# Kernel optimization log

Measured on AMD Instinct MI355X. Metric: run time of the kernel, lower is better.

## Reference

```python
import jax, jax.numpy as jnp
import numpy as np

DIM = 64     # qudit dimension (size of M)
WIRES = 3    # total qudits; full Hilbert dim D = DIM**WIRES = 262144
INDEX = 1    # wire the custom gate acts on
BATCH = 128  # number of state columns


def setup_inputs() -> dict:
    key = jax.random.key(0)
    k1, k2, k3, k4 = jax.random.split(key, 4)
    D = DIM ** WIRES
    return {
        "M_real": jax.random.normal(k1, (DIM, DIM), dtype=jnp.float32),
        "M_imag": jax.random.normal(k2, (DIM, DIM), dtype=jnp.float32),
        "x_real": jax.random.normal(k3, (D, BATCH), dtype=jnp.float32),
        "x_imag": jax.random.normal(k4, (D, BATCH), dtype=jnp.float32),
    }


def reference(M_real, M_imag, x_real, x_imag):
    # Original torch code builds U = I_{dim^index} (x) M (x) I_{dim^(wires-index-1)}
    # via iterative kron, then computes U @ x. Mathematically identical and
    # exponentially cheaper: reshape x to expose the target qudit axis and
    # contract M only along that axis (tensor-network style).
    M = jax.lax.complex(M_real, M_imag)          # (dim, dim) complex64
    x = jax.lax.complex(x_real, x_imag)          # (D, B) complex64
    B = x.shape[1]
    left = DIM ** INDEX                          # dims before target wire
    right = DIM ** (WIRES - INDEX - 1)           # dims after target wire
    xr = x.reshape(left, DIM, right, B)          # (a, j, r, b)
    y = jnp.einsum('ij,ajrb->airb', M, xr)       # apply M on the target axis
    return y.reshape(DIM ** WIRES, B)            # same as (kron U) @ x
```

## Files before the change

kernel.cpp:

```cpp
#include <hip/hip_runtime.h>

#define DIMQ   64
#define NCOLS  8192
#define SLAB   (DIMQ * NCOLS)
#define NA     64
#define DB     (NA * SLAB)

#define NT     128
#define TILES  8
#define NCG    8

typedef __attribute__((ext_vector_type(8))) __bf16 bf16x8;
typedef __attribute__((ext_vector_type(8))) unsigned short us8;
typedef __attribute__((ext_vector_type(4))) unsigned short us4;
typedef __attribute__((ext_vector_type(4))) float f32x4;

__device__ __forceinline__ unsigned short f2bf(float f) {
    unsigned u = __builtin_bit_cast(unsigned, f);
    unsigned r = u + 0x7fffu + ((u >> 16) & 1u);
    return (unsigned short)(r >> 16);
}

__device__ __forceinline__ int xsw(int row, int chunk) {
    return chunk ^ ((row >> 2) & 7) ^ ((row & 3) << 1);
}

__global__ __launch_bounds__(512, 4) void gate_real_kernel(
    const float* __restrict__ Mr, const float* __restrict__ Mi,
    const float* __restrict__ Xr, const float* __restrict__ Xi,
    float* __restrict__ Out)
{
    __shared__ alignas(16) unsigned char smem[32768];
    unsigned short* ldsX = (unsigned short*)smem;
    float* ldsO = (float*)smem;

    const int tid  = threadIdx.x;
    const int lane = tid & 63;
    const int w    = tid >> 6;
    const int l15  = lane & 15;
    const int q    = lane >> 4;
    const int it   = w & 3;
    const int nh   = w >> 2;

    const int a  = blockIdx.x >> 3;
    const int cg = blockIdx.x & 7;
    const size_t baseA = (size_t)a * SLAB;
    const int ncg0 = cg * (TILES * NT);

    bf16x8 fMr[2], fMni[2];
#pragma unroll
    for (int kb = 0; kb < 2; ++kb) {
        const int row = it * 16 + l15;
        const int col = kb * 32 + q * 8;
        const float* pr = Mr + row * DIMQ + col;
        const float* pi = Mi + row * DIMQ + col;
        us8 hr, hni;
#pragma unroll
        for (int j = 0; j < 8; ++j) {
            hr[j]  = f2bf(pr[j]);
            hni[j] = (unsigned short)(f2bf(pi[j]) ^ 0x8000u);
        }
        fMr[kb]  = __builtin_bit_cast(bf16x8, hr);
        fMni[kb] = __builtin_bit_cast(bf16x8, hni);
    }

    const int k0    = (tid >> 5) * 4;
    const int sn    = (tid & 31) * 4;
    const int chunk = k0 >> 3;
    const int ko4   = k0 & 4;

    f32x4 vr[4], vi[4];
    {
        const float* gr = Xr + baseA + (size_t)k0 * NCOLS + ncg0 + sn;
        const float* gi = Xi + baseA + (size_t)k0 * NCOLS + ncg0 + sn;
#pragma unroll
        for (int j = 0; j < 4; ++j)
            vr[j] = *reinterpret_cast<const f32x4*>(gr + (size_t)j * NCOLS);
#pragma unroll
        for (int j = 0; j < 4; ++j)
            vi[j] = *reinterpret_cast<const f32x4*>(gi + (size_t)j * NCOLS);
    }

    for (int t = 0; t < TILES; ++t) {
#pragma unroll
        for (int z = 0; z < 4; ++z) {
            const int row = sn + z;
            const int e   = row * 64 + xsw(row, chunk) * 8 + ko4;
            us4 hr, hi;
#pragma unroll
            for (int j = 0; j < 4; ++j) {
                hr[j] = f2bf(vr[j][z]);
                hi[j] = f2bf(vi[j][z]);
            }
            *reinterpret_cast<us4*>(&ldsX[e])        = hr;
            *reinterpret_cast<us4*>(&ldsX[8192 + e]) = hi;
        }

        if (t + 1 < TILES) {
            const float* gr = Xr + baseA + (size_t)k0 * NCOLS + ncg0 + (t + 1) * NT + sn;
            const float* gi = Xi + baseA + (size_t)k0 * NCOLS + ncg0 + (t + 1) * NT + sn;
#pragma unroll
            for (int j = 0; j < 4; ++j)
                vr[j] = *reinterpret_cast<const f32x4*>(gr + (size_t)j * NCOLS);
#pragma unroll
            for (int j = 0; j < 4; ++j)
                vi[j] = *reinterpret_cast<const f32x4*>(gi + (size_t)j * NCOLS);
        }
        __syncthreads();

        f32x4 acc[4];
#pragma unroll
        for (int nt = 0; nt < 4; ++nt) acc[nt] = f32x4{0, 0, 0, 0};
#pragma unroll
        for (int nt = 0; nt < 4; ++nt) {
#pragma unroll
            for (int kb = 0; kb < 2; ++kb) {
                const int row = (nh * 4 + nt) * 16 + l15;
                const int e   = row * 64 + xsw(row, kb * 4 + q) * 8;
                const bf16x8 bXr = __builtin_bit_cast(bf16x8,
                    *reinterpret_cast<const us8*>(&ldsX[e]));
                const bf16x8 bXi = __builtin_bit_cast(bf16x8,
                    *reinterpret_cast<const us8*>(&ldsX[8192 + e]));
                acc[nt] = __builtin_amdgcn_mfma_f32_16x16x32_bf16(fMr[kb],  bXr, acc[nt], 0, 0, 0);
                acc[nt] = __builtin_amdgcn_mfma_f32_16x16x32_bf16(fMni[kb], bXi, acc[nt], 0, 0, 0);
            }
        }
        __syncthreads();

#pragma unroll
        for (int nt = 0; nt < 4; ++nt) {
#pragma unroll
            for (int r = 0; r < 4; ++r) {
                const int row = it * 16 + q * 4 + r;
                const int col = nh * 64 + nt * 16 + l15;
                ldsO[row * 128 + (col ^ ((row & 7) << 2))] = acc[nt][r];
            }
        }
        __syncthreads();

        {
            const int ci = (tid & 31) * 4;
            const int r0 = tid >> 5;
            const int n0 = ncg0 + t * NT;
#pragma unroll
            for (int p = 0; p < 4; ++p) {
                const int row = p * 16 + r0;
                const int d   = ci ^ ((row & 7) << 2);
                const f32x4 v = *reinterpret_cast<const f32x4*>(&ldsO[row * 128 + d]);
                *reinterpret_cast<f32x4*>(Out + baseA + (size_t)row * NCOLS + n0 + ci) = v;
            }
        }
        __syncthreads();
    }
}

__device__ __forceinline__ void load_M_frags_full(
    const float* __restrict__ Mr, const float* __restrict__ Mi,
    int l15, int q, bf16x8 fMr[4][2], bf16x8 fMi[4][2])
{
#pragma unroll
    for (int it = 0; it < 4; ++it) {
#pragma unroll
        for (int kb = 0; kb < 2; ++kb) {
            const int row = it * 16 + l15;
            const int col = kb * 32 + q * 8;
            const float* pr = Mr + row * DIMQ + col;
            const float* pi = Mi + row * DIMQ + col;
            us8 hr, hi;
#pragma unroll
            for (int j = 0; j < 8; ++j) {
                hr[j] = f2bf(pr[j]);
                hi[j] = f2bf(pi[j]);
            }
            fMr[it][kb] = __builtin_bit_cast(bf16x8, hr);
            fMi[it][kb] = __builtin_bit_cast(bf16x8, hi);
        }
    }
}

__global__ __launch_bounds__(64, 2) void gate_cplx_kernel(
    const float* __restrict__ Mr, const float* __restrict__ Mi,
    const float* __restrict__ Xr, const float* __restrict__ Xi,
    float* __restrict__ Out)
{
    const int lane = threadIdx.x;
    const int l15  = lane & 15;
    const int q    = lane >> 4;

    bf16x8 fMr[4][2], fMi[4][2];
    load_M_frags_full(Mr, Mi, l15, q, fMr, fMi);

    const int bid = blockIdx.x;
    const int a   = bid >> 6;
    const int nch = bid & 63;
    const size_t baseA = (size_t)a * SLAB;

    for (int tt = 0; tt < 8; ++tt) {
        const int n0 = nch * 128 + tt * 16;
        f32x4 accR[4] = {f32x4{0,0,0,0}, f32x4{0,0,0,0}, f32x4{0,0,0,0}, f32x4{0,0,0,0}};
        f32x4 accI[4] = {f32x4{0,0,0,0}, f32x4{0,0,0,0}, f32x4{0,0,0,0}, f32x4{0,0,0,0}};

#pragma unroll
        for (int kb = 0; kb < 2; ++kb) {
            const int krow = kb * 32 + q * 8;
            const float* pr = Xr + baseA + (size_t)krow * NCOLS + n0 + l15;
            const float* pi = Xi + baseA + (size_t)krow * NCOLS + n0 + l15;
            float fr[8], fi[8];
#pragma unroll
            for (int j = 0; j < 8; ++j) {
                fr[j] = pr[(size_t)j * NCOLS];
                fi[j] = pi[(size_t)j * NCOLS];
            }
            us8 hr, hi, hni;
#pragma unroll
            for (int j = 0; j < 8; ++j) {
                hr[j] = f2bf(fr[j]);
                const unsigned short tbf = f2bf(fi[j]);
                hi[j]  = tbf;
                hni[j] = (unsigned short)(tbf ^ 0x8000u);
            }
            const bf16x8 bXr  = __builtin_bit_cast(bf16x8, hr);
            const bf16x8 bXi  = __builtin_bit_cast(bf16x8, hi);
            const bf16x8 bXni = __builtin_bit_cast(bf16x8, hni);

#pragma unroll
            for (int it = 0; it < 4; ++it) {
                accR[it] = __builtin_amdgcn_mfma_f32_16x16x32_bf16(fMr[it][kb], bXr,  accR[it], 0, 0, 0);
                accR[it] = __builtin_amdgcn_mfma_f32_16x16x32_bf16(fMi[it][kb], bXni, accR[it], 0, 0, 0);
                accI[it] = __builtin_amdgcn_mfma_f32_16x16x32_bf16(fMr[it][kb], bXi,  accI[it], 0, 0, 0);
                accI[it] = __builtin_amdgcn_mfma_f32_16x16x32_bf16(fMi[it][kb], bXr,  accI[it], 0, 0, 0);
            }
        }

#pragma unroll
        for (int it = 0; it < 4; ++it) {
#pragma unroll
            for (int r = 0; r < 4; ++r) {
                const int i = it * 16 + q * 4 + r;
                const size_t cidx = baseA + (size_t)i * NCOLS + n0 + l15;
                float2 v;
                v.x = accR[it][r];
                v.y = accI[it][r];
                reinterpret_cast<float2*>(Out)[cidx] = v;
            }
        }
    }
}

extern "C" void kernel_launch(void* const* d_in, const int* in_sizes, int n_in,
                              void* d_out, int out_size, void* d_ws, size_t ws_size,
                              hipStream_t stream) {
    const float* Mr = (const float*)d_in[0];
    const float* Mi = (const float*)d_in[1];
    const float* Xr = (const float*)d_in[2];
    const float* Xi = (const float*)d_in[3];
    float* Out = (float*)d_out;

    if (out_size >= 2 * DB) {
        dim3 grid(NA * 64);
        dim3 block(64);
        gate_cplx_kernel<<<grid, block, 0, stream>>>(Mr, Mi, Xr, Xi, Out);
    } else {
        dim3 grid(NA * NCG);
        dim3 block(512);
        gate_real_kernel<<<grid, block, 0, stream>>>(Mr, Mi, Xr, Xi, Out);
    }
}
```

Baseline: 319.0 us.

## Double-buffer X tiles in LDS and halve column tile per block

Halves the column tile size and doubles the number of column groups per slab, so more blocks run in parallel. The X staging buffer is now double-buffered in LDS with a separate output buffer, which lets the store of the previous tile overlap with the conversion and load of the next. Synchronisation drops from four barriers to two per tile, and each barrier waits only on LDS counters. Real and imaginary loads are split across the two halves of the block. The cost is more LDS per block (about 48KB), which may cut the number of resident blocks per CU.

Result: no change. 316.8 us (-0.7%).

```diff
diff --git a/kernel.cpp b/kernel.cpp
--- a/kernel.cpp
+++ b/kernel.cpp
@@ -6,9 +6,9 @@
 #define NA     64
 #define DB     (NA * SLAB)
 
-#define NT     128
+#define NT     64
 #define TILES  8
-#define NCG    8
+#define NCG    16
 
 typedef __attribute__((ext_vector_type(8))) __bf16 bf16x8;
 typedef __attribute__((ext_vector_type(8))) unsigned short us8;
@@ -24,15 +24,19 @@
 __device__ __forceinline__ int xsw(int row, int chunk) {
     return chunk ^ ((row >> 2) & 7) ^ ((row & 3) << 1);
 }
+
+#define BARRIER() do { \
+    asm volatile("s_waitcnt lgkmcnt(0)" ::: "memory"); \
+    __builtin_amdgcn_s_barrier(); \
+} while (0)
 
 __global__ __launch_bounds__(512, 4) void gate_real_kernel(
     const float* __restrict__ Mr, const float* __restrict__ Mi,
     const float* __restrict__ Xr, const float* __restrict__ Xi,
     float* __restrict__ Out)
 {
-    __shared__ alignas(16) unsigned char smem[32768];
-    unsigned short* ldsX = (unsigned short*)smem;
-    float* ldsO = (float*)smem;
+    __shared__ alignas(16) unsigned short ldsX[2][2][64 * 64];
+    __shared__ alignas(16) float ldsO[64 * 64];
 
     const int tid  = threadIdx.x;
     const int lane = tid & 63;
@@ -40,10 +44,10 @@
     const int l15  = lane & 15;
     const int q    = lane >> 4;
     const int it   = w & 3;
-    const int nh   = w >> 2;
-
-    const int a  = blockIdx.x >> 3;
-    const int cg = blockIdx.x & 7;
+    const int nh   = (w >> 2) & 1;
+
+    const int a  = blockIdx.x >> 4;
+    const int cg = blockIdx.x & 15;
     const size_t baseA = (size_t)a * SLAB;
     const int ncg0 = cg * (TILES * NT);
 
@@ -64,94 +68,114 @@
         fMni[kb] = __builtin_bit_cast(bf16x8, hni);
     }
 
-    const int k0    = (tid >> 5) * 4;
-    const int sn    = (tid & 31) * 4;
-    const int chunk = k0 >> 3;
-    const int ko4   = k0 & 4;
-
-    f32x4 vr[4], vi[4];
-    {
-        const float* gr = Xr + baseA + (size_t)k0 * NCOLS + ncg0 + sn;
-        const float* gi = Xi + baseA + (size_t)k0 * NCOLS + ncg0 + sn;
+    const int c  = tid >> 8;
+    const int k0 = ((tid >> 4) & 15) * 4;
+    const int sn = (tid & 15) * 4;
+    const float* Xc = c ? Xi : Xr;
+    const float* gbase = Xc + baseA + (size_t)k0 * NCOLS + ncg0 + sn;
+
+    f32x4 vA[4], vB[4];
+
+    auto LOADT = [&](f32x4 v[4], int t) {
+        const float* g = gbase + (size_t)t * NT;
 #pragma unroll
         for (int j = 0; j < 4; ++j)
-            vr[j] = *reinterpret_cast<const f32x4*>(gr + (size_t)j * NCOLS);
-#pragma unroll
-        for (int j = 0; j < 4; ++j)
-            vi[j] = *reinterpret_cast<const f32x4*>(gi + (size_t)j * NCOLS);
-    }
-
-    for (int t = 0; t < TILES; ++t) {
+            v[j] = *reinterpret_cast<const f32x4*>(g + (size_t)j * NCOLS);
+    };
+
+    auto XWRITE = [&](const f32x4 v[4], int buf) {
+        unsigned short* L = &ldsX[buf][c][0];
+        const int chunk = k0 >> 3;
+        const int ko4   = k0 & 4;
 #pragma unroll
         for (int z = 0; z < 4; ++z) {
             const int row = sn + z;
             const int e   = row * 64 + xsw(row, chunk) * 8 + ko4;
-            us4 hr, hi;
-#pragma unroll
-            for (int j = 0; j < 4; ++j) {
-                hr[j] = f2bf(vr[j][z]);
-                hi[j] = f2bf(vi[j][z]);
-            }
-            *reinterpret_cast<us4*>(&ldsX[e])        = hr;
-            *reinterpret_cast<us4*>(&ldsX[8192 + e]) = hi;
-        }
-
-        if (t + 1 < TILES) {
-            const float* gr = Xr + baseA + (size_t)k0 * NCOLS + ncg0 + (t + 1) * NT + sn;
-            const float* gi = Xi + baseA + (size_t)k0 * NCOLS + ncg0 + (t + 1) * NT + sn;
-#pragma unroll
-            for (int j = 0; j < 4; ++j)
-                vr[j] = *reinterpret_cast<const f32x4*>(gr + (size_t)j * NCOLS);
-#pragma unroll
-            for (int j = 0; j < 4; ++j)
-                vi[j] = *reinterpret_cast<const f32x4*>(gi + (size_t)j * NCOLS);
-        }
-        __syncthreads();
-
-        f32x4 acc[4];
-#pragma unroll
-        for (int nt = 0; nt < 4; ++nt) acc[nt] = f32x4{0, 0, 0, 0};
-#pragma unroll
-        for (int nt = 0; nt < 4; ++nt) {
+            us4 h;
+#pragma unroll
+            for (int j = 0; j < 4; ++j) h[j] = f2bf(v[j][z]);
+            *reinterpret_cast<us4*>(&L[e]) = h;
+        }
+    };
+
+    auto COMPUTE = [&](int buf, f32x4 acc[2]) {
+        acc[0] = f32x4{0, 0, 0, 0};
+        acc[1] = f32x4{0, 0, 0, 0};
+#pragma unroll
+        for (int nt = 0; nt < 2; ++nt) {
 #pragma unroll
             for (int kb = 0; kb < 2; ++kb) {
-                const int row = (nh * 4 + nt) * 16 + l15;
+                const int row = nh * 32 + nt * 16 + l15;
                 const int e   = row * 64 + xsw(row, kb * 4 + q) * 8;
                 const bf16x8 bXr = __builtin_bit_cast(bf16x8,
-                    *reinterpret_cast<const us8*>(&ldsX[e]));
+                    *reinterpret_cast<const us8*>(&ldsX[buf][0][e]));
                 const bf16x8 bXi = __builtin_bit_cast(bf16x8,
-                    *reinterpret_cast<const us8*>(&ldsX[8192 + e]));
+                    *reinterpret_cast<const us8*>(&ldsX[buf][1][e]));
                 acc[nt] = __builtin_amdgcn_mfma_f32_16x16x32_bf16(fMr[kb],  bXr, acc[nt], 0, 0, 0);
                 acc[nt] = __builtin_amdgcn_mfma_f32_16x16x32_bf16(fMni[kb], bXi, acc[nt], 0, 0, 0);
             }
         }
-        __syncthreads();
-
-#pragma unroll
-        for (int nt = 0; nt < 4; ++nt) {
+    };
+
+    auto OWRITE = [&](const f32x4 acc[2]) {
+#pragma unroll
+        for (int nt = 0; nt < 2; ++nt) {
 #pragma unroll
             for (int r = 0; r < 4; ++r) {
                 const int row = it * 16 + q * 4 + r;
-                const int col = nh * 64 + nt * 16 + l15;
-                ldsO[row * 128 + (col ^ ((row & 7) << 2))] = acc[nt][r];
-            }
-        }
-        __syncthreads();
-
-        {
-            const int ci = (tid & 31) * 4;
-            const int r0 = tid >> 5;
-            const int n0 = ncg0 + t * NT;
-#pragma unroll
-            for (int p = 0; p < 4; ++p) {
-                const int row = p * 16 + r0;
-                const int d   = ci ^ ((row & 7) << 2);
-                const f32x4 v = *reinterpret_cast<const f32x4*>(&ldsO[row * 128 + d]);
-                *reinterpret_cast<f32x4*>(Out + baseA + (size_t)row * NCOLS + n0 + ci) = v;
-            }
-        }
-        __syncthreads();
-    }
+                const int col = nh * 32 + nt * 16 + l15;
+                ldsO[row * 64 + (col ^ ((row & 7) << 2))] = acc[nt][r];
+            }
+        }
+    };
+
+    auto OSTORE = [&](int t) {
+        const int ci = (tid & 15) * 4;
+        const int r0 = tid >> 4;
+        const int n0 = ncg0 + t * NT;
+#pragma unroll
+        for (int p = 0; p < 2; ++p) {
+            const int row = p * 32 + r0;
+            const int d   = ci ^ ((row & 7) << 2);
+            const f32x4 v = *reinterpret_cast<const f32x4*>(&ldsO[row * 64 + d]);
+            *reinterpret_cast<f32x4*>(Out + baseA + (size_t)row * NCOLS + n0 + ci) = v;
+        }
+    };
+
+    f32x4 acc[2];
+
+    LOADT(vA, 0);
+    XWRITE(vA, 0);
+    LOADT(vB, 1);
+    BARRIER();
+    COMPUTE(0, acc);
+    OWRITE(acc);
+    BARRIER();
+
+    for (int t = 1; t < TILES - 1; t += 2) {
+        OSTORE(t - 1);
+        XWRITE(vB, 1);
+        LOADT(vA, t + 1);
+        BARRIER();
+        COMPUTE(1, acc);
+        OWRITE(acc);
+        BARRIER();
+        OSTORE(t);
+        XWRITE(vA, 0);
+        if (t + 2 < TILES) LOADT(vB, t + 2);
+        BARRIER();
+        COMPUTE(0, acc);
+        OWRITE(acc);
+        BARRIER();
+    }
+
+    OSTORE(TILES - 2);
+    XWRITE(vB, 1);
+    BARRIER();
+    COMPUTE(1, acc);
+    OWRITE(acc);
+    BARRIER();
+    OSTORE(TILES - 1);
 }
 
 __device__ __forceinline__ void load_M_frags_full(
```
